# Performance work log

Measured on AMD Instinct MI355X. Metric: run time of the kernel, lower is better.

The kernel has to match this reference:

```python
import jax, jax.numpy as jnp
import numpy as np

EPS = 1e-6

def _rms_norm(x, w):
    # normalize over last dim (head_dim)
    var = jnp.mean(jnp.square(x), axis=-1, keepdims=True)
    return x * jax.lax.rsqrt(var + EPS) * w

def _rotate_half(x):
    half = x.shape[-1] // 2
    first, second = x[..., :half], x[..., half:]
    return jnp.concatenate([-second, first], axis=-1)

def _apply_rope(x, cos, sin):
    # x: [B,H,S,D]; cos/sin: [B,S,D] -> broadcast over heads
    return x * cos[:, None] + _rotate_half(x) * sin[:, None]

def setup_inputs() -> dict:
    key = jax.random.key(0)
    ks = jax.random.split(key, 10)
    B, Sq, Sk, Dm, H = 2, 2048, 2048, 2048, 16
    hd = Dm // H
    scale = 1.0 / np.sqrt(Dm)
    return {
        "x": jax.random.normal(ks[0], (B, Sq, Dm), jnp.float32),
        "context": jax.random.normal(ks[1], (B, Sk, Dm), jnp.float32),
        "cos_q": jax.random.uniform(ks[2], (B, Sq, hd), jnp.float32),
        "sin_q": jax.random.uniform(ks[3], (B, Sq, hd), jnp.float32),
        "cos_k": jax.random.uniform(ks[4], (B, Sk, hd), jnp.float32),
        "sin_k": jax.random.uniform(ks[5], (B, Sk, hd), jnp.float32),
        "Wq": jax.random.normal(ks[6], (Dm, Dm), jnp.float32) * scale,
        "Wk": jax.random.normal(ks[7], (Dm, Dm), jnp.float32) * scale,
        "Wv": jax.random.normal(ks[8], (Dm, Dm), jnp.float32) * scale,
        "Wo": jax.random.normal(ks[9], (Dm, Dm), jnp.float32) * scale,
        "q_norm_w": jnp.ones((hd,), jnp.float32),
        "k_norm_w": jnp.ones((hd,), jnp.float32),
    }

def reference(x, context, cos_q, sin_q, cos_k, sin_k, Wq, Wk, Wv, Wo, q_norm_w, k_norm_w):
    B, Sq, Dm = x.shape
    hd = q_norm_w.shape[0]
    H = Dm // hd
    # projections (torch Linear: y = x @ W.T), reshape to [B,H,S,D]
    q = (x @ Wq.T).reshape(B, Sq, H, hd).transpose(0, 2, 1, 3)
    k = (context @ Wk.T).reshape(B, -1, H, hd).transpose(0, 2, 1, 3)
    v = (context @ Wv.T).reshape(B, -1, H, hd).transpose(0, 2, 1, 3)
    # per-head QK RMSNorm
    q = _rms_norm(q, q_norm_w)
    k = _rms_norm(k, k_norm_w)
    # RoPE
    q = _apply_rope(q, cos_q, sin_q)
    k = _apply_rope(k, cos_k, sin_k)
    # SDPA, scale = 1/sqrt(head_dim)
    scale = 1.0 / np.sqrt(hd).astype(np.float32)
    scores = jnp.einsum('bhqd,bhkd->bhqk', q, k) * scale
    attn = jax.nn.softmax(scores, axis=-1)
    y = jnp.einsum('bhqk,bhkd->bhqd', attn, v)
    y = y.transpose(0, 2, 1, 3).reshape(B, Sq, Dm)
    return y @ Wo.T
```

## Files before the change

kernel.cpp:

```cpp
#include <hip/hip_runtime.h>


typedef __attribute__((ext_vector_type(8))) short bf16x8;
typedef __attribute__((ext_vector_type(4))) float f32x4;

#define AS1(p) ((__attribute__((address_space(1))) void*)(p))
#define AS3(p) ((__attribute__((address_space(3))) void*)(p))
#define STG(g, l) __builtin_amdgcn_global_load_lds(AS1(g), AS3(l), 16, 0, 0)

__device__ __forceinline__ unsigned short f2bf(float f) {
  unsigned int u = __float_as_uint(f);
  u += 0x7fffu + ((u >> 16) & 1u);
  return (unsigned short)(u >> 16);
}
__device__ __forceinline__ float bf2f(unsigned short u) {
  return __uint_as_float(((unsigned int)u) << 16);
}

constexpr int B_ = 2, S_ = 2048, DM = 2048, H_ = 16, HD = 128;
constexpr int M_ = B_ * S_;

__global__ __launch_bounds__(256) void castbf(const float* __restrict__ X,
                                              unsigned short* __restrict__ Y, int n4) {
  int i = blockIdx.x * 256 + threadIdx.x;
  if (i >= n4) return;
  float4 v = ((const float4*)X)[i];
  ushort4 u;
  u.x = f2bf(v.x); u.y = f2bf(v.y); u.z = f2bf(v.z); u.w = f2bf(v.w);
  ((ushort4*)Y)[i] = u;
}

template <int BF16OUT>
__device__ __forceinline__ void gemm_core(const unsigned short* __restrict__ A,
                                          const unsigned short* __restrict__ Bw,
                                          void* __restrict__ Cv,
                                          unsigned short* lds) {
  const int tid = threadIdx.x, wave = tid >> 6, lane = tid & 63;
  const int quad = lane >> 4, l16 = lane & 15;
  const int m0 = blockIdx.x * 128, n0 = blockIdx.y * 256;
  const int wn = wave * 64;
  constexpr int NT = DM / 32;
  constexpr int SLOT = 12288;

  f32x4 acc[8][4];
#pragma unroll
  for (int f = 0; f < 8; f++)
#pragma unroll
    for (int g = 0; g < 4; g++) acc[f][g] = (f32x4){0.f, 0.f, 0.f, 0.f};

  const unsigned short* srcA[2];
  const unsigned short* srcB[4];
#pragma unroll
  for (int i = 0; i < 2; i++) {
    int c = tid + i * 256, L = c >> 3, ph = c & 7, j = ph ^ (L & 7);
    srcA[i] = A + (size_t)(m0 + L + ((j >> 2) << 6)) * DM + (j & 3) * 8;
  }
#pragma unroll
  for (int i = 0; i < 4; i++) {
    int c = tid + i * 256, L = c >> 3, ph = c & 7, j = ph ^ (L & 7);
    srcB[i] = Bw + (size_t)(n0 + L + ((j >> 2) << 7)) * DM + (j & 3) * 8;
  }

#define STAGE_H0(T, S)                                                         \
  { const int ko = (T) << 5; unsigned short* lb = lds + (S) * SLOT + wave * 512;\
    STG(srcA[0] + ko, lb);                                                     \
    STG(srcA[1] + ko, lb + 2048);                                              \
    STG(srcB[0] + ko, lb + 4096); }
#define STAGE_H1(T, S)                                                         \
  { const int ko = (T) << 5; unsigned short* lb = lds + (S) * SLOT + wave * 512;\
    STG(srcB[1] + ko, lb + 6144);                                              \
    STG(srcB[2] + ko, lb + 8192);                                              \
    STG(srcB[3] + ko, lb + 10240); }

  const int x8 = l16 & 7;
  const int ab0 = l16 * 64 + ((quad ^ x8)) * 8;
  const int ab1 = l16 * 64 + (((4 | quad) ^ x8)) * 8;
  const int bb  = 4096 + (wn & 64) * 64 + l16 * 64 +
                  ((((wave >> 1) << 2) | quad) ^ x8) * 8;

  STAGE_H0(0, 0) STAGE_H1(0, 0)
  STAGE_H0(1, 1) STAGE_H1(1, 1)
  asm volatile("s_waitcnt vmcnt(6)" ::: "memory");
  __builtin_amdgcn_s_barrier();

  int st = 0, s2 = 2;
  for (int t = 0; t < NT; ++t) {
    const unsigned short* ls = lds + st * SLOT;

    bf16x8 af0[4], bfv[4];
#pragma unroll
    for (int f = 0; f < 4; f++) af0[f] = *(const bf16x8*)(ls + f * 1024 + ab0);
#pragma unroll
    for (int g = 0; g < 4; g++) bfv[g] = *(const bf16x8*)(ls + g * 1024 + bb);
    if (t + 2 < NT) STAGE_H0(t + 2, s2)
    __builtin_amdgcn_s_barrier();
    __builtin_amdgcn_s_setprio(1);
#pragma unroll
    for (int f = 0; f < 4; f++)
#pragma unroll
      for (int g = 0; g < 4; g++)
        acc[f][g] = __builtin_amdgcn_mfma_f32_16x16x32_bf16(af0[f], bfv[g], acc[f][g], 0, 0, 0);
    __builtin_amdgcn_s_setprio(0);
    __builtin_amdgcn_s_barrier();

    bf16x8 af1[4];
#pragma unroll
    for (int f = 0; f < 4; f++) af1[f] = *(const bf16x8*)(ls + f * 1024 + ab1);
    if (t + 2 < NT) STAGE_H1(t + 2, s2)
    if (t < NT - 2)       asm volatile("s_waitcnt vmcnt(6)" ::: "memory");
    else if (t == NT - 2) asm volatile("s_waitcnt vmcnt(0)" ::: "memory");
    __builtin_amdgcn_s_barrier();
    __builtin_amdgcn_s_setprio(1);
#pragma unroll
    for (int f = 0; f < 4; f++)
#pragma unroll
      for (int g = 0; g < 4; g++)
        acc[f + 4][g] = __builtin_amdgcn_mfma_f32_16x16x32_bf16(af1[f], bfv[g], acc[f + 4][g], 0, 0, 0);
    __builtin_amdgcn_s_setprio(0);
    if (t < NT - 1) __builtin_amdgcn_s_barrier();

    st++; if (st == 3) st = 0;
    s2++; if (s2 == 3) s2 = 0;
  }
#undef STAGE_H0
#undef STAGE_H1

#pragma unroll
  for (int f = 0; f < 8; f++)
#pragma unroll
    for (int g = 0; g < 4; g++) {
      const size_t row = (size_t)(m0 + f * 16 + quad * 4);
      const int col = n0 + wn + g * 16 + l16;
      if (BF16OUT) {
        unsigned short* cp = (unsigned short*)Cv + row * DM + col;
#pragma unroll
        for (int r = 0; r < 4; r++) cp[(size_t)r * DM] = f2bf(acc[f][g][r]);
      } else {
        float* cp = (float*)Cv + row * DM + col;
#pragma unroll
        for (int r = 0; r < 4; r++) cp[(size_t)r * DM] = acc[f][g][r];
      }
    }
}

__global__ __launch_bounds__(256, 2) void gemm_qkv(const unsigned short* __restrict__ xb,
                                                   const unsigned short* __restrict__ cb,
                                                   const unsigned short* __restrict__ Wq,
                                                   const unsigned short* __restrict__ Wk,
                                                   const unsigned short* __restrict__ Wv,
                                                   unsigned short* __restrict__ Pq,
                                                   unsigned short* __restrict__ Pk,
                                                   unsigned short* __restrict__ Pv) {
  __shared__ __align__(16) unsigned short lds[3 * 12288];
  const int z = blockIdx.z;
  const unsigned short* A  = (z == 0) ? xb : cb;
  const unsigned short* Bw = (z == 0) ? Wq : (z == 1) ? Wk : Wv;
  unsigned short* C        = (z == 0) ? Pq : (z == 1) ? Pk : Pv;
  gemm_core<1>(A, Bw, C, lds);
}

__global__ __launch_bounds__(256, 2) void gemm_bt(const unsigned short* __restrict__ A,
                                                  const unsigned short* __restrict__ Bw,
                                                  float* __restrict__ C) {
  __shared__ __align__(16) unsigned short lds[3 * 12288];
  gemm_core<0>(A, Bw, C, lds);
}

__global__ __launch_bounds__(256) void normrope(const unsigned short* __restrict__ X,
                                                const float* __restrict__ Cs,
                                                const float* __restrict__ Sn,
                                                const float* __restrict__ W,
                                                unsigned short* __restrict__ Out,
                                                float scale) {
  int gw = (blockIdx.x * 256 + threadIdx.x) >> 6;
  int lane = threadIdx.x & 63;
  int h = gw & 15, bs = gw >> 4;
  int s = bs & (S_ - 1), b = bs >> 11;
  const unsigned short* xr = X + (size_t)gw * HD;
  float x0 = bf2f(xr[lane]), x1 = bf2f(xr[lane + 64]);
  float ss = x0 * x0 + x1 * x1;
#pragma unroll
  for (int off = 32; off > 0; off >>= 1) ss += __shfl_xor(ss, off);
  float rr = rsqrtf(ss * (1.0f / 128.0f) + 1e-6f);
  float n0 = x0 * rr * W[lane], n1 = x1 * rr * W[lane + 64];
  const float* cp = Cs + (size_t)bs * HD;
  const float* sp = Sn + (size_t)bs * HD;
  float o0 = (n0 * cp[lane] - n1 * sp[lane]) * scale;
  float o1 = (n1 * cp[lane + 64] + n0 * sp[lane + 64]) * scale;
  unsigned short* orow = Out + (((size_t)(b * H_ + h)) * S_ + s) * HD;
  orow[lane] = f2bf(o0);
  orow[lane + 64] = f2bf(o1);
}

__global__ __launch_bounds__(256) void vtrans(const unsigned short* __restrict__ Vf,
                                              unsigned short* __restrict__ Vt) {
  __shared__ unsigned short tile[128 * 72];
  const int tid = threadIdx.x;
  const int sc = blockIdx.x & 31;
  const int bh = blockIdx.x >> 5;
  const int b = bh >> 4, h = bh & 15;
  const int s0 = sc * 64;
#pragma unroll
  for (int it = 0; it < 4; ++it) {
    int ci = it * 256 + tid;
    int s = ci >> 4, dc = ci & 15;
    bf16x8 v = *(const bf16x8*)(Vf + ((size_t)(b * S_ + s0 + s)) * DM + h * HD + dc * 8);
    unsigned short* tp = tile + (dc * 8) * 72 + s;
#pragma unroll
    for (int e = 0; e < 8; e++) tp[e * 72] = (unsigned short)v[e];
  }
  __syncthreads();
#pragma unroll
  for (int it = 0; it < 4; ++it) {
    int cj = it * 256 + tid;
    int d = cj >> 3, scx = cj & 7;
    bf16x8 vv = *(const bf16x8*)(tile + d * 72 + scx * 8);
    *(bf16x8*)(Vt + ((size_t)bh * HD + d) * S_ + s0 + scx * 8) = vv;
  }
}

__global__ __launch_bounds__(256, 2) void flash(const unsigned short* __restrict__ Q,
                                                const unsigned short* __restrict__ Kt,
                                                const unsigned short* __restrict__ Vt,
                                                unsigned short* __restrict__ Y) {
  __shared__ unsigned short lK[2 * 64 * HD];
  __shared__ unsigned short lV[2 * HD * 64];
  __shared__ unsigned short lP[4 * 1024];
  const int tid = threadIdx.x, wave = tid >> 6, lane = tid & 63;
  const int quad = lane >> 4, l16 = lane & 15;
  const int qb = blockIdx.x & 15;
  const int bh = blockIdx.x >> 4;
  const int b = bh >> 4, h = bh & 15;
  const int q0 = qb * 128 + wave * 32;

  bf16x8 aq[2][4];
#pragma unroll
  for (int u = 0; u < 2; u++) {
    const unsigned short* qrow = Q + ((size_t)bh * S_ + q0 + u * 16 + l16) * HD;
#pragma unroll
    for (int t = 0; t < 4; t++) aq[u][t] = *(const bf16x8*)(qrow + t * 32 + quad * 8);
  }
  f32x4 o[2][8];
#pragma unroll
  for (int u = 0; u < 2; u++)
#pragma unroll
    for (int t = 0; t < 8; t++) o[u][t] = (f32x4){0.f, 0.f, 0.f, 0.f};
  float lsum[2][4] = {{0.f, 0.f, 0.f, 0.f}, {0.f, 0.f, 0.f, 0.f}};

  const unsigned short* kbase = Kt + (size_t)bh * S_ * HD;
  const unsigned short* vbase = Vt + (size_t)bh * HD * S_;
  unsigned short* lPw = lP + wave * 1024;
  const int mrow = quad * 4;
  const int xsl = (l16 >> 1) & 3;
  const int xsl7 = (l16 >> 1) & 7;

#define STAGEKV(K0, BUF)                                                       \
  {                                                                            \
    const unsigned short* kb_ = kbase + (size_t)(K0) * HD;                     \
    const unsigned short* vb_ = vbase + (K0);                                  \
    _Pragma("unroll")                                                          \
    for (int call = 0; call < 4; ++call) {                                     \
      int c = call * 256 + tid;                         \
      int key = c >> 4, sk = c & 15;           \
      int dck = sk ^ (key & 15);                                               \
      STG(kb_ + (size_t)key * HD + dck * 8,                                    \
          lK + (BUF) * 8192 + (call * 256 + wave * 64) * 8);                   \
      int dv = c >> 3, sv = c & 7;             \
      int kc = sv ^ ((dv >> 1) & 7);                                           \
      STG(vb_ + (size_t)dv * S_ + kc * 8,                                      \
          lV + (BUF) * 8192 + (call * 256 + wave * 64) * 8);                   \
    }                                                                          \
  }

  STAGEKV(0, 0)

  for (int it = 0; it < S_ / 64; ++it) {
    if (it + 1 < S_ / 64) {
      STAGEKV((it + 1) * 64, (it + 1) & 1)
      asm volatile("s_waitcnt vmcnt(8)" ::: "memory");
    } else {
      asm volatile("s_waitcnt vmcnt(0)" ::: "memory");
    }
    __builtin_amdgcn_s_barrier();

    const unsigned short* lKc = lK + (it & 1) * 8192;
    const unsigned short* lVc = lV + (it & 1) * 8192;

#pragma unroll
    for (int h2 = 0; h2 < 2; ++h2) {
      f32x4 s0[2] = {(f32x4){0.f, 0.f, 0.f, 0.f}, (f32x4){0.f, 0.f, 0.f, 0.f}};
      f32x4 s1[2] = {(f32x4){0.f, 0.f, 0.f, 0.f}, (f32x4){0.f, 0.f, 0.f, 0.f}};
      {
        const unsigned short* krow0 = lKc + (h2 * 32 + l16) * HD;
        const unsigned short* krow1 = krow0 + 16 * HD;
        __builtin_amdgcn_s_setprio(1);
#pragma unroll
        for (int t = 0; t < 4; t++) {
          int dcq = t * 4 + quad;
          bf16x8 kf0 = *(const bf16x8*)(krow0 + (dcq ^ l16) * 8);
          bf16x8 kf1 = *(const bf16x8*)(krow1 + (dcq ^ l16) * 8);
#pragma unroll
          for (int u = 0; u < 2; u++) {
            s0[u] = __builtin_amdgcn_mfma_f32_16x16x32_bf16(aq[u][t], kf0, s0[u], 0, 0, 0);
            s1[u] = __builtin_amdgcn_mfma_f32_16x16x32_bf16(aq[u][t], kf1, s1[u], 0, 0, 0);
          }
        }
        __builtin_amdgcn_s_setprio(0);
      }
#pragma unroll
      for (int u = 0; u < 2; u++) {
        unsigned short* lPu = lPw + u * 512;
#pragma unroll
        for (int r = 0; r < 4; r++) {
          int m = mrow + r;
          int sx = (m >> 1) & 3;
          float p0 = __expf(s0[u][r]);
          float p1 = __expf(s1[u][r]);
          lsum[u][r] += p0 + p1;
          int kc0 = l16 >> 3;
          lPu[m * 32 + ((kc0 ^ sx)) * 8 + (l16 & 7)] = f2bf(p0);
          lPu[m * 32 + (((kc0 + 2) ^ sx)) * 8 + (l16 & 7)] = f2bf(p1);
        }
      }
      bf16x8 pf[2];
#pragma unroll
      for (int u = 0; u < 2; u++)
        pf[u] = *(const bf16x8*)(lPw + u * 512 + l16 * 32 + (quad ^ xsl) * 8);
      __builtin_amdgcn_s_setprio(1);
#pragma unroll
      for (int t = 0; t < 8; t++) {
        bf16x8 vf = *(const bf16x8*)(lVc + (t * 16 + l16) * 64 + ((h2 * 4 + quad) ^ xsl7) * 8);
#pragma unroll
        for (int u = 0; u < 2; u++)
          o[u][t] = __builtin_amdgcn_mfma_f32_16x16x32_bf16(pf[u], vf, o[u][t], 0, 0, 0);
      }
      __builtin_amdgcn_s_setprio(0);
    }

    __builtin_amdgcn_s_barrier();
  }
#undef STAGEKV

#pragma unroll
  for (int off = 1; off < 16; off <<= 1) {
#pragma unroll
    for (int u = 0; u < 2; u++)
#pragma unroll
      for (int r = 0; r < 4; r++) lsum[u][r] += __shfl_xor(lsum[u][r], off);
  }
  float inv[2][4];
#pragma unroll
  for (int u = 0; u < 2; u++)
#pragma unroll
    for (int r = 0; r < 4; r++) inv[u][r] = 1.0f / lsum[u][r];
#pragma unroll
  for (int u = 0; u < 2; u++)
#pragma unroll
    for (int t = 0; t < 8; t++)
#pragma unroll
      for (int r = 0; r < 4; r++) {
        size_t idx = ((size_t)b * S_ + q0 + u * 16 + mrow + r) * DM + h * HD + t * 16 + l16;
        Y[idx] = f2bf(o[u][t][r] * inv[u][r]);
      }
}

extern "C" void kernel_launch(void* const* d_in, const int* in_sizes, int n_in,
                              void* d_out, int out_size, void* d_ws, size_t ws_size,
                              hipStream_t stream) {
  const float* x    = (const float*)d_in[0];
  const float* ctx  = (const float*)d_in[1];
  const float* cosq = (const float*)d_in[2];
  const float* sinq = (const float*)d_in[3];
  const float* cosk = (const float*)d_in[4];
  const float* sink = (const float*)d_in[5];
  const float* Wq   = (const float*)d_in[6];
  const float* Wk   = (const float*)d_in[7];
  const float* Wv   = (const float*)d_in[8];
  const float* Wo   = (const float*)d_in[9];
  const float* qw   = (const float*)d_in[10];
  const float* kw   = (const float*)d_in[11];

  char* ws = (char*)d_ws;
  const size_t ACT2 = (size_t)M_ * DM * 2;
  const size_t W2   = (size_t)DM * DM * 2;
  unsigned short* xb  = (unsigned short*)(ws);
  unsigned short* cb  = (unsigned short*)(ws + ACT2);
  unsigned short* Wqb = (unsigned short*)(ws + 2 * ACT2);
  unsigned short* Wkb = (unsigned short*)(ws + 2 * ACT2 + W2);
  unsigned short* Wvb = (unsigned short*)(ws + 2 * ACT2 + 2 * W2);
  unsigned short* Wob = (unsigned short*)(ws + 2 * ACT2 + 3 * W2);
  unsigned short* Pq  = (unsigned short*)(ws + 2 * ACT2 + 4 * W2);
  unsigned short* Pk  = (unsigned short*)(ws + 3 * ACT2 + 4 * W2);
  unsigned short* Pv  = (unsigned short*)(ws + 4 * ACT2 + 4 * W2);
  unsigned short* qn = xb;
  unsigned short* kn = Wqb;
  unsigned short* vt = cb;
  unsigned short* yb = Pq;

  const float scale = 0.0883883476483184f;

  castbf<<<M_ * DM / 1024, 256, 0, stream>>>(x, xb, M_ * DM / 4);
  castbf<<<M_ * DM / 1024, 256, 0, stream>>>(ctx, cb, M_ * DM / 4);
  castbf<<<DM * DM / 1024, 256, 0, stream>>>(Wq, Wqb, DM * DM / 4);
  castbf<<<DM * DM / 1024, 256, 0, stream>>>(Wk, Wkb, DM * DM / 4);
  castbf<<<DM * DM / 1024, 256, 0, stream>>>(Wv, Wvb, DM * DM / 4);
  castbf<<<DM * DM / 1024, 256, 0, stream>>>(Wo, Wob, DM * DM / 4);

  dim3 gq(M_ / 128, DM / 256, 3);
  gemm_qkv<<<gq, 256, 0, stream>>>(xb, cb, Wqb, Wkb, Wvb, Pq, Pk, Pv);

  normrope<<<M_ * H_ / 4, 256, 0, stream>>>(Pq, cosq, sinq, qw, qn, scale);
  normrope<<<M_ * H_ / 4, 256, 0, stream>>>(Pk, cosk, sink, kw, kn, 1.0f);
  vtrans<<<B_ * H_ * (S_ / 64), 256, 0, stream>>>(Pv, vt);

  flash<<<B_ * H_ * (S_ / 128), 256, 0, stream>>>(qn, kn, vt, yb);

  dim3 gg(M_ / 128, DM / 256);
  gemm_bt<<<gg, 256, 0, stream>>>(yb, Wob, (float*)d_out);

  (void)in_sizes; (void)n_in; (void)out_size; (void)ws_size;
}
```

Baseline: 455.8 us.

## Enlarge GEMM tiles to 256x256 with 8 waves and fuse cast kernels

The GEMM core now uses 256x256 output tiles with 512 threads (8 waves arranged 2x4), and the LDS staging, swizzle offsets and wait counts are restructured to match. Each loaded tile is reused by more output, which cuts global/L2 traffic per FLOP. The six separate fp32-to-bf16 cast launches are merged into a single kernel to save launch overhead. In exchange the grid has half as many blocks (fewer waves across the CUs), LDS use per block is larger, and the 2-blocks-per-CU launch bound at 512 threads may raise register pressure.

```diff
diff --git a/kernel.cpp b/kernel.cpp
--- a/kernel.cpp
+++ b/kernel.cpp
@@ -20,14 +20,32 @@
 constexpr int B_ = 2, S_ = 2048, DM = 2048, H_ = 16, HD = 128;
 constexpr int M_ = B_ * S_;
 
-__global__ __launch_bounds__(256) void castbf(const float* __restrict__ X,
-                                              unsigned short* __restrict__ Y, int n4) {
+__global__ __launch_bounds__(256) void castall(const float* __restrict__ x,
+                                               const float* __restrict__ ctx,
+                                               const float* __restrict__ Wq,
+                                               const float* __restrict__ Wk,
+                                               const float* __restrict__ Wv,
+                                               const float* __restrict__ Wo,
+                                               unsigned short* __restrict__ xb,
+                                               unsigned short* __restrict__ cb,
+                                               unsigned short* __restrict__ Wqb,
+                                               unsigned short* __restrict__ Wkb,
+                                               unsigned short* __restrict__ Wvb,
+                                               unsigned short* __restrict__ Wob) {
+  constexpr int A4 = M_ * DM / 4;
+  constexpr int W4 = DM * DM / 4;
   int i = blockIdx.x * 256 + threadIdx.x;
-  if (i >= n4) return;
-  float4 v = ((const float4*)X)[i];
+  const float* src; unsigned short* dst; int off;
+  if (i < A4)                { src = x;   dst = xb;  off = i; }
+  else if (i < 2 * A4)       { src = ctx; dst = cb;  off = i - A4; }
+  else if (i < 2 * A4 + W4)  { src = Wq;  dst = Wqb; off = i - 2 * A4; }
+  else if (i < 2 * A4 + 2 * W4) { src = Wk; dst = Wkb; off = i - 2 * A4 - W4; }
+  else if (i < 2 * A4 + 3 * W4) { src = Wv; dst = Wvb; off = i - 2 * A4 - 2 * W4; }
+  else                       { src = Wo;  dst = Wob; off = i - 2 * A4 - 3 * W4; }
+  float4 v = ((const float4*)src)[off];
   ushort4 u;
   u.x = f2bf(v.x); u.y = f2bf(v.y); u.z = f2bf(v.z); u.w = f2bf(v.w);
-  ((ushort4*)Y)[i] = u;
+  ((ushort4*)dst)[off] = u;
 }
 
 template <int BF16OUT>
@@ -37,10 +55,10 @@
                                           unsigned short* lds) {
   const int tid = threadIdx.x, wave = tid >> 6, lane = tid & 63;
   const int quad = lane >> 4, l16 = lane & 15;
-  const int m0 = blockIdx.x * 128, n0 = blockIdx.y * 256;
-  const int wn = wave * 64;
+  const int m0 = blockIdx.x * 256, n0 = blockIdx.y * 256;
+  const int wm = (wave >> 2) * 128, wn = (wave & 3) * 64;
   constexpr int NT = DM / 32;
-  constexpr int SLOT = 12288;
+  constexpr int SLOT = 16384;
 
   f32x4 acc[8][4];
 #pragma unroll
@@ -49,38 +67,33 @@
     for (int g = 0; g < 4; g++) acc[f][g] = (f32x4){0.f, 0.f, 0.f, 0.f};
 
   const unsigned short* srcA[2];
-  const unsigned short* srcB[4];
+  const unsigned short* srcB[2];
+  int wst[2];
 #pragma unroll
   for (int i = 0; i < 2; i++) {
-    int c = tid + i * 256, L = c >> 3, ph = c & 7, j = ph ^ (L & 7);
-    srcA[i] = A + (size_t)(m0 + L + ((j >> 2) << 6)) * DM + (j & 3) * 8;
-  }
-#pragma unroll
-  for (int i = 0; i < 4; i++) {
-    int c = tid + i * 256, L = c >> 3, ph = c & 7, j = ph ^ (L & 7);
+    int c = tid + i * 512, L = c >> 3, ph = c & 7, j = ph ^ (L & 7);
+    srcA[i] = A + (size_t)(m0 + L + ((j >> 2) << 7)) * DM + (j & 3) * 8;
     srcB[i] = Bw + (size_t)(n0 + L + ((j >> 2) << 7)) * DM + (j & 3) * 8;
-  }
-
-#define STAGE_H0(T, S)                                                         \
-  { const int ko = (T) << 5; unsigned short* lb = lds + (S) * SLOT + wave * 512;\
-    STG(srcA[0] + ko, lb);                                                     \
-    STG(srcA[1] + ko, lb + 2048);                                              \
-    STG(srcB[0] + ko, lb + 4096); }
-#define STAGE_H1(T, S)                                                         \
-  { const int ko = (T) << 5; unsigned short* lb = lds + (S) * SLOT + wave * 512;\
-    STG(srcB[1] + ko, lb + 6144);                                              \
-    STG(srcB[2] + ko, lb + 8192);                                              \
-    STG(srcB[3] + ko, lb + 10240); }
+    wst[i] = (i * 512 + wave * 64) * 8;
+  }
+
+#define STAGE_A(T, S)                                                          \
+  { const int ko = (T) << 5;                                                   \
+    STG(srcA[0] + ko, lds + (S) * SLOT + wst[0]);                              \
+    STG(srcA[1] + ko, lds + (S) * SLOT + wst[1]); }
+#define STAGE_B(T, S)                                                          \
+  { const int ko = (T) << 5;                                                   \
+    STG(srcB[0] + ko, lds + (S) * SLOT + 8192 + wst[0]);                       \
+    STG(srcB[1] + ko, lds + (S) * SLOT + 8192 + wst[1]); }
 
   const int x8 = l16 & 7;
-  const int ab0 = l16 * 64 + ((quad ^ x8)) * 8;
-  const int ab1 = l16 * 64 + (((4 | quad) ^ x8)) * 8;
-  const int bb  = 4096 + (wn & 64) * 64 + l16 * 64 +
-                  ((((wave >> 1) << 2) | quad) ^ x8) * 8;
-
-  STAGE_H0(0, 0) STAGE_H1(0, 0)
-  STAGE_H0(1, 1) STAGE_H1(1, 1)
-  asm volatile("s_waitcnt vmcnt(6)" ::: "memory");
+  const int abase = l16 * 64 + ((((wave >> 2) << 2) | quad) ^ x8) * 8;
+  const int bbase = 8192 + (wn & 64) * 64 + l16 * 64 +
+                    ((((wave >> 1) & 1) << 2 | quad) ^ x8) * 8;
+
+  STAGE_A(0, 0) STAGE_B(0, 0)
+  STAGE_A(1, 1) STAGE_B(1, 1)
+  asm volatile("s_waitcnt vmcnt(4)" ::: "memory");
   __builtin_amdgcn_s_barrier();
 
   int st = 0, s2 = 2;
@@ -89,10 +102,10 @@
 
     bf16x8 af0[4], bfv[4];
 #pragma unroll
-    for (int f = 0; f < 4; f++) af0[f] = *(const bf16x8*)(ls + f * 1024 + ab0);
-#pragma unroll
-    for (int g = 0; g < 4; g++) bfv[g] = *(const bf16x8*)(ls + g * 1024 + bb);
-    if (t + 2 < NT) STAGE_H0(t + 2, s2)
+    for (int f = 0; f < 4; f++) af0[f] = *(const bf16x8*)(ls + f * 1024 + abase);
+#pragma unroll
+    for (int g = 0; g < 4; g++) bfv[g] = *(const bf16x8*)(ls + g * 1024 + bbase);
+    if (t + 2 < NT) STAGE_A(t + 2, s2)
     __builtin_amdgcn_s_barrier();
     __builtin_amdgcn_s_setprio(1);
 #pragma unroll
@@ -105,9 +118,9 @@
 
     bf16x8 af1[4];
 #pragma unroll
-    for (int f = 0; f < 4; f++) af1[f] = *(const bf16x8*)(ls + f * 1024 + ab1);
-    if (t + 2 < NT) STAGE_H1(t + 2, s2)
-    if (t < NT - 2)       asm volatile("s_waitcnt vmcnt(6)" ::: "memory");
+    for (int f = 0; f < 4; f++) af1[f] = *(const bf16x8*)(ls + (f + 4) * 1024 + abase);
+    if (t + 2 < NT) STAGE_B(t + 2, s2)
+    if (t < NT - 2)       asm volatile("s_waitcnt vmcnt(4)" ::: "memory");
     else if (t == NT - 2) asm volatile("s_waitcnt vmcnt(0)" ::: "memory");
     __builtin_amdgcn_s_barrier();
     __builtin_amdgcn_s_setprio(1);
@@ -122,14 +135,14 @@
     st++; if (st == 3) st = 0;
     s2++; if (s2 == 3) s2 = 0;
   }
-#undef STAGE_H0
-#undef STAGE_H1
+#undef STAGE_A
+#undef STAGE_B
 
 #pragma unroll
   for (int f = 0; f < 8; f++)
 #pragma unroll
     for (int g = 0; g < 4; g++) {
-      const size_t row = (size_t)(m0 + f * 16 + quad * 4);
+      const size_t row = (size_t)(m0 + wm + f * 16 + quad * 4);
       const int col = n0 + wn + g * 16 + l16;
       if (BF16OUT) {
         unsigned short* cp = (unsigned short*)Cv + row * DM + col;
@@ -143,7 +156,7 @@
     }
 }
 
-__global__ __launch_bounds__(256, 2) void gemm_qkv(const unsigned short* __restrict__ xb,
+__global__ __launch_bounds__(512, 2) void gemm_qkv(const unsigned short* __restrict__ xb,
                                                    const unsigned short* __restrict__ cb,
                                                    const unsigned short* __restrict__ Wq,
                                                    const unsigned short* __restrict__ Wk,
@@ -151,7 +164,7 @@
                                                    unsigned short* __restrict__ Pq,
                                                    unsigned short* __restrict__ Pk,
                                                    unsigned short* __restrict__ Pv) {
-  __shared__ __align__(16) unsigned short lds[3 * 12288];
+  __shared__ __align__(16) unsigned short lds[3 * 16384];
   const int z = blockIdx.z;
   const unsigned short* A  = (z == 0) ? xb : cb;
   const unsigned short* Bw = (z == 0) ? Wq : (z == 1) ? Wk : Wv;
@@ -159,10 +172,10 @@
   gemm_core<1>(A, Bw, C, lds);
 }
 
-__global__ __launch_bounds__(256, 2) void gemm_bt(const unsigned short* __restrict__ A,
+__global__ __launch_bounds__(512, 2) void gemm_bt(const unsigned short* __restrict__ A,
                                                   const unsigned short* __restrict__ Bw,
                                                   float* __restrict__ C) {
-  __shared__ __align__(16) unsigned short lds[3 * 12288];
+  __shared__ __align__(16) unsigned short lds[3 * 16384];
   gemm_core<0>(A, Bw, C, lds);
 }
 
@@ -399,15 +412,11 @@
 
   const float scale = 0.0883883476483184f;
 
-  castbf<<<M_ * DM / 1024, 256, 0, stream>>>(x, xb, M_ * DM / 4);
-  castbf<<<M_ * DM / 1024, 256, 0, stream>>>(ctx, cb, M_ * DM / 4);
-  castbf<<<DM * DM / 1024, 256, 0, stream>>>(Wq, Wqb, DM * DM / 4);
-  castbf<<<DM * DM / 1024, 256, 0, stream>>>(Wk, Wkb, DM * DM / 4);
-  castbf<<<DM * DM / 1024, 256, 0, stream>>>(Wv, Wvb, DM * DM / 4);
-  castbf<<<DM * DM / 1024, 256, 0, stream>>>(Wo, Wob, DM * DM / 4);
-
-  dim3 gq(M_ / 128, DM / 256, 3);
-  gemm_qkv<<<gq, 256, 0, stream>>>(xb, cb, Wqb, Wkb, Wvb, Pq, Pk, Pv);
+  castall<<<(2 * M_ * DM + 4 * DM * DM) / 1024, 256, 0, stream>>>(
+      x, ctx, Wq, Wk, Wv, Wo, xb, cb, Wqb, Wkb, Wvb, Wob);
+
+  dim3 gq(M_ / 256, DM / 256, 3);
+  gemm_qkv<<<gq, 512, 0, stream>>>(xb, cb, Wqb, Wkb, Wvb, Pq, Pk, Pv);
 
   normrope<<<M_ * H_ / 4, 256, 0, stream>>>(Pq, cosq, sinq, qw, qn, scale);
   normrope<<<M_ * H_ / 4, 256, 0, stream>>>(Pk, cosk, sink, kw, kn, 1.0f);
@@ -415,8 +424,8 @@
 
   flash<<<B_ * H_ * (S_ / 128), 256, 0, stream>>>(qn, kn, vt, yb);
 
-  dim3 gg(M_ / 128, DM / 256);
-  gemm_bt<<<gg, 256, 0, stream>>>(yb, Wob, (float*)d_out);
+  dim3 gg(M_ / 256, DM / 256);
+  gemm_bt<<<gg, 512, 0, stream>>>(yb, Wob, (float*)d_out);
 
   (void)in_sizes; (void)n_in; (void)out_size; (void)ws_size;
 }
```

Result: slower. 478.0 us (+4.9%).

## Merge cast and prep launches, split-K output projection with add kernel

Applied to the files above, without the earlier changes.

Folds the six fp32-to-bf16 cast launches into one kernel, and the two normrope launches plus the V transpose into one prep kernel, to cut launch overhead and tail gaps. The output projection GEMM becomes split-K with two K halves along grid z. Each half writes an fp32 partial into workspace, and a separate add kernel sums them into the output. The split-K doubles the grid to fill more CUs, at the cost of extra fp32 partial writes and reads plus one more launch.

```diff
diff --git a/kernel.cpp b/kernel.cpp
--- a/kernel.cpp
+++ b/kernel.cpp
@@ -20,17 +20,35 @@
 constexpr int B_ = 2, S_ = 2048, DM = 2048, H_ = 16, HD = 128;
 constexpr int M_ = B_ * S_;
 
-__global__ __launch_bounds__(256) void castbf(const float* __restrict__ X,
-                                              unsigned short* __restrict__ Y, int n4) {
+__global__ __launch_bounds__(256) void castall(const float* __restrict__ x,
+                                               const float* __restrict__ ctx,
+                                               const float* __restrict__ Wq,
+                                               const float* __restrict__ Wk,
+                                               const float* __restrict__ Wv,
+                                               const float* __restrict__ Wo,
+                                               unsigned short* __restrict__ xb,
+                                               unsigned short* __restrict__ cb,
+                                               unsigned short* __restrict__ Wqb,
+                                               unsigned short* __restrict__ Wkb,
+                                               unsigned short* __restrict__ Wvb,
+                                               unsigned short* __restrict__ Wob) {
+  constexpr int A4 = M_ * DM / 4;
+  constexpr int W4 = DM * DM / 4;
   int i = blockIdx.x * 256 + threadIdx.x;
-  if (i >= n4) return;
-  float4 v = ((const float4*)X)[i];
+  const float* src; unsigned short* dst; int off;
+  if (i < A4)                { src = x;   dst = xb;  off = i; }
+  else if (i < 2 * A4)       { src = ctx; dst = cb;  off = i - A4; }
+  else if (i < 2 * A4 + W4)  { src = Wq;  dst = Wqb; off = i - 2 * A4; }
+  else if (i < 2 * A4 + 2 * W4) { src = Wk; dst = Wkb; off = i - 2 * A4 - W4; }
+  else if (i < 2 * A4 + 3 * W4) { src = Wv; dst = Wvb; off = i - 2 * A4 - 2 * W4; }
+  else                       { src = Wo;  dst = Wob; off = i - 2 * A4 - 3 * W4; }
+  float4 v = ((const float4*)src)[off];
   ushort4 u;
   u.x = f2bf(v.x); u.y = f2bf(v.y); u.z = f2bf(v.z); u.w = f2bf(v.w);
-  ((ushort4*)Y)[i] = u;
-}
-
-template <int BF16OUT>
+  ((ushort4*)dst)[off] = u;
+}
+
+template <int BF16OUT, int NT>
 __device__ __forceinline__ void gemm_core(const unsigned short* __restrict__ A,
                                           const unsigned short* __restrict__ Bw,
                                           void* __restrict__ Cv,
@@ -39,7 +57,6 @@
   const int quad = lane >> 4, l16 = lane & 15;
   const int m0 = blockIdx.x * 128, n0 = blockIdx.y * 256;
   const int wn = wave * 64;
-  constexpr int NT = DM / 32;
   constexpr int SLOT = 12288;
 
   f32x4 acc[8][4];
@@ -156,23 +173,36 @@
   const unsigned short* A  = (z == 0) ? xb : cb;
   const unsigned short* Bw = (z == 0) ? Wq : (z == 1) ? Wk : Wv;
   unsigned short* C        = (z == 0) ? Pq : (z == 1) ? Pk : Pv;
-  gemm_core<1>(A, Bw, C, lds);
+  gemm_core<1, 64>(A, Bw, C, lds);
 }
 
 __global__ __launch_bounds__(256, 2) void gemm_bt(const unsigned short* __restrict__ A,
                                                   const unsigned short* __restrict__ Bw,
-                                                  float* __restrict__ C) {
+                                                  float* __restrict__ C1,
+                                                  float* __restrict__ C2) {
   __shared__ __align__(16) unsigned short lds[3 * 12288];
-  gemm_core<0>(A, Bw, C, lds);
-}
-
-__global__ __launch_bounds__(256) void normrope(const unsigned short* __restrict__ X,
-                                                const float* __restrict__ Cs,
-                                                const float* __restrict__ Sn,
-                                                const float* __restrict__ W,
-                                                unsigned short* __restrict__ Out,
-                                                float scale) {
-  int gw = (blockIdx.x * 256 + threadIdx.x) >> 6;
+  const int z = blockIdx.z;
+  gemm_core<0, 32>(A + (z << 10), Bw + (z << 10),
+                   z ? (void*)C2 : (void*)C1, lds);
+}
+
+__global__ __launch_bounds__(256) void addout(const float4* __restrict__ a,
+                                              const float4* __restrict__ b,
+                                              float4* __restrict__ o, int n4) {
+  int i = blockIdx.x * 256 + threadIdx.x;
+  if (i >= n4) return;
+  float4 x = a[i], y = b[i];
+  o[i] = make_float4(x.x + y.x, x.y + y.y, x.z + y.z, x.w + y.w);
+}
+
+__device__ __forceinline__ void normrope_body(int bid,
+                                              const unsigned short* __restrict__ X,
+                                              const float* __restrict__ Cs,
+                                              const float* __restrict__ Sn,
+                                              const float* __restrict__ W,
+                                              unsigned short* __restrict__ Out,
+                                              float scale) {
+  int gw = (bid * 256 + threadIdx.x) >> 6;
   int lane = threadIdx.x & 63;
   int h = gw & 15, bs = gw >> 4;
   int s = bs & (S_ - 1), b = bs >> 11;
@@ -192,12 +222,13 @@
   orow[lane + 64] = f2bf(o1);
 }
 
-__global__ __launch_bounds__(256) void vtrans(const unsigned short* __restrict__ Vf,
-                                              unsigned short* __restrict__ Vt) {
-  __shared__ unsigned short tile[128 * 72];
+__device__ __forceinline__ void vtrans_body(int bid,
+                                            const unsigned short* __restrict__ Vf,
+                                            unsigned short* __restrict__ Vt,
+                                            unsigned short* tile) {
   const int tid = threadIdx.x;
-  const int sc = blockIdx.x & 31;
-  const int bh = blockIdx.x >> 5;
+  const int sc = bid & 31;
+  const int bh = bid >> 5;
   const int b = bh >> 4, h = bh & 15;
   const int s0 = sc * 64;
 #pragma unroll
@@ -217,6 +248,27 @@
     bf16x8 vv = *(const bf16x8*)(tile + d * 72 + scx * 8);
     *(bf16x8*)(Vt + ((size_t)bh * HD + d) * S_ + s0 + scx * 8) = vv;
   }
+}
+
+__global__ __launch_bounds__(256) void prep(const unsigned short* __restrict__ Pq,
+                                            const unsigned short* __restrict__ Pk,
+                                            const unsigned short* __restrict__ Pv,
+                                            const float* __restrict__ cq,
+                                            const float* __restrict__ sq,
+                                            const float* __restrict__ ck,
+                                            const float* __restrict__ sk,
+                                            const float* __restrict__ qw,
+                                            const float* __restrict__ kw,
+                                            unsigned short* __restrict__ qn,
+                                            unsigned short* __restrict__ kn,
+                                            unsigned short* __restrict__ vt,
+                                            float scale) {
+  __shared__ unsigned short tile[128 * 72];
+  constexpr int NR = M_ * H_ / 4;
+  int bx = blockIdx.x;
+  if (bx < NR)            normrope_body(bx, Pq, cq, sq, qw, qn, scale);
+  else if (bx < 2 * NR)   normrope_body(bx - NR, Pk, ck, sk, kw, kn, 1.0f);
+  else                    vtrans_body(bx - 2 * NR, Pv, vt, tile);
 }
 
 __global__ __launch_bounds__(256, 2) void flash(const unsigned short* __restrict__ Q,
@@ -396,27 +448,27 @@
   unsigned short* kn = Wqb;
   unsigned short* vt = cb;
   unsigned short* yb = Pq;
+  float* C1 = (float*)Pk;
+  float* C2 = (float*)xb;
 
   const float scale = 0.0883883476483184f;
 
-  castbf<<<M_ * DM / 1024, 256, 0, stream>>>(x, xb, M_ * DM / 4);
-  castbf<<<M_ * DM / 1024, 256, 0, stream>>>(ctx, cb, M_ * DM / 4);
-  castbf<<<DM * DM / 1024, 256, 0, stream>>>(Wq, Wqb, DM * DM / 4);
-  castbf<<<DM * DM / 1024, 256, 0, stream>>>(Wk, Wkb, DM * DM / 4);
-  castbf<<<DM * DM / 1024, 256, 0, stream>>>(Wv, Wvb, DM * DM / 4);
-  castbf<<<DM * DM / 1024, 256, 0, stream>>>(Wo, Wob, DM * DM / 4);
+  castall<<<(2 * M_ * DM + 4 * DM * DM) / 1024, 256, 0, stream>>>(
+      x, ctx, Wq, Wk, Wv, Wo, xb, cb, Wqb, Wkb, Wvb, Wob);
 
   dim3 gq(M_ / 128, DM / 256, 3);
   gemm_qkv<<<gq, 256, 0, stream>>>(xb, cb, Wqb, Wkb, Wvb, Pq, Pk, Pv);
 
-  normrope<<<M_ * H_ / 4, 256, 0, stream>>>(Pq, cosq, sinq, qw, qn, scale);
-  normrope<<<M_ * H_ / 4, 256, 0, stream>>>(Pk, cosk, sink, kw, kn, 1.0f);
-  vtrans<<<B_ * H_ * (S_ / 64), 256, 0, stream>>>(Pv, vt);
+  prep<<<2 * (M_ * H_ / 4) + B_ * H_ * (S_ / 64), 256, 0, stream>>>(
+      Pq, Pk, Pv, cosq, sinq, cosk, sink, qw, kw, qn, kn, vt, scale);
 
   flash<<<B_ * H_ * (S_ / 128), 256, 0, stream>>>(qn, kn, vt, yb);
 
-  dim3 gg(M_ / 128, DM / 256);
-  gemm_bt<<<gg, 256, 0, stream>>>(yb, Wob, (float*)d_out);
+  dim3 gg(M_ / 128, DM / 256, 2);
+  gemm_bt<<<gg, 256, 0, stream>>>(yb, Wob, C1, C2);
+
+  addout<<<M_ * DM / 1024, 256, 0, stream>>>((const float4*)C1, (const float4*)C2,
+                                             (float4*)d_out, M_ * DM / 4);
 
   (void)in_sizes; (void)n_in; (void)out_size; (void)ws_size;
 }
```

After: 454.3 us. About the same (-0.3%).
